# Kernel tuning notes

Hardware: AMD Instinct MI355X
Metric: run time of the kernel (lower is better)

The kernel has to match this reference:

```python
import jax, jax.numpy as jnp
import numpy as np

K = 3        # prediction_steps
SKIP = 1     # skip_step (forward default)
NEG = 64     # opt.negative_samples
EPS = 1e-11  # ExpNLLLoss epsilon


def setup_inputs() -> dict:
    key = jax.random.key(0)
    ks = jax.random.split(key, 8)
    B, C, H, W = 64, 256, 14, 14
    z = jax.random.normal(ks[0], (B, C, H, W), jnp.float32)
    c = jax.random.normal(ks[1], (B, C, H, W), jnp.float32)
    Wk = jax.random.normal(ks[2], (K, C, C), jnp.float32) / np.sqrt(C).astype(np.float32)
    inp = {"z": z, "c": c, "Wk": Wk}
    for k in range(1, K + 1):
        Hp = H - (k + SKIP)
        rows = Hp * W * B
        inp[f"neg_idx_k{k}"] = jax.random.randint(ks[2 + k], (rows * NEG,), 0, rows, dtype=jnp.int32)
    return inp


def _loss_k(z, c, Wk, neg_idx, k):
    # z, c: [B,C,H,W]; Wk: [Co,Ci] (1x1 conv); neg_idx: [(H-k-SKIP)*W*B*NEG]
    B, C, H, W = z.shape
    Hp = H - (k + SKIP)
    zt = z[:, :, k + SKIP:, :]                            # [B,Ci,Hp,W]
    ztwk = jnp.einsum('oc,bchw->hwbo', Wk, zt)            # [Hp,W,B,Co] (1x1 conv + permute(2,3,0,1))
    flat = ztwk.reshape(Hp * W * B, -1)
    shuf = flat[neg_idx].reshape(Hp, W, B, NEG, -1)       # gathered negatives [Hp,W,B,N,Co]
    ctx = jnp.transpose(c[:, :, :Hp, :], (2, 3, 0, 1))    # context c[:,:,:-(k+SKIP),:] -> [Hp,W,B,Co]
    main = jnp.einsum('hwbc,hwbc->hwb', ctx, ztwk)[..., None]   # [Hp,W,B,1]
    negs = jnp.einsum('hwbc,hwbnc->hwbn', ctx, shuf)            # [Hp,W,B,N]
    log_fk = jnp.concatenate([main, negs], axis=-1)             # [Hp,W,B,1+N]
    log_fk = jnp.transpose(log_fk, (2, 3, 0, 1))                # [B,1+N,Hp,W]
    probs = jax.nn.softmax(log_fk, axis=1)
    # ExpNLLLoss, target class 0, reduction='mean'
    return -jnp.mean(jnp.log(probs[:, 0] + EPS))


def reference(z, c, Wk, neg_idx_k1, neg_idx_k2, neg_idx_k3):
    idxs = [neg_idx_k1, neg_idx_k2, neg_idx_k3]
    total = 0.0
    for k in range(1, K + 1):
        total = total + _loss_k(z, c, Wk[k - 1], idxs[k - 1], k)
    return total / K
```

## Files before the change

kernel.cpp:

```cpp
#include <hip/hip_runtime.h>
#include <math.h>


typedef short bf16x8 __attribute__((ext_vector_type(8)));
typedef float f32x4 __attribute__((ext_vector_type(4)));

static __device__ __forceinline__ unsigned short f2bf(float f) {
    union { float f; unsigned int u; } x; x.f = f;
    unsigned int r = x.u + 0x7fffu + ((x.u >> 16) & 1u);
    return (unsigned short)(r >> 16);
}

static __device__ __forceinline__ unsigned char f2e4m3(float f) {
    union { float f; unsigned int u; } x; x.f = f;
    unsigned int s = (x.u >> 24) & 0x80u;
    float af = fabsf(f);
    if (af > 448.f) af = 448.f;
    x.f = af;
    unsigned int u = x.u;
    int e = (int)(u >> 23) - 127;
    unsigned int out;
    if (af == 0.f) {
        out = 0u;
    } else if (e < -6) {
        int mq = (int)rintf(af * 512.f);
        out = (mq >= 8) ? 0x08u : (unsigned int)mq;
    } else {
        unsigned int r = u + 0x7FFFFu + ((u >> 20) & 1u);
        int e2 = (int)(r >> 23) - 127;
        if (e2 > 8) out = 0x7Eu;
        else out = (unsigned int)(((e2 + 7) << 3) | ((r >> 20) & 7u));
    }
    return (unsigned char)(s | out);
}

static __device__ __forceinline__ void gload_lds4(const void* g, void* l) {
    __builtin_amdgcn_global_load_lds(
        (const __attribute__((address_space(1))) void*)g,
        (__attribute__((address_space(3))) void*)l, 4, 0, 0);
}

__global__ __launch_bounds__(256)
void prep_kernel(const float* __restrict__ z, const float* __restrict__ c,
                 const float* __restrict__ Wk,
                 unsigned short* __restrict__ zt, unsigned char* __restrict__ ct8,
                 unsigned short* __restrict__ wkb, float* __restrict__ out) {
    __shared__ float tile[16][201];
    const int tid = threadIdx.x;
    int x = blockIdx.x;
    if (x < 768) {
        int i = x * 256 + tid;
        wkb[i] = f2bf(Wk[i]);
        if (x == 0 && tid == 0) out[0] = 0.f;
        return;
    }
    const bool isz = x < 1792;
    const int local = isz ? (x - 768) : (x - 1792);
    const float* src = isz ? z : c;
    const int b  = local & 63;
    const int c0 = (local >> 6) << 4;
    for (int i = tid; i < 16 * 196; i += 256) {
        int cc = i / 196;
        int hw = i - cc * 196;
        tile[cc][hw] = src[(size_t)((b << 8) + c0 + cc) * 196 + hw];
    }
    __syncthreads();
    if (isz) {
        for (int i = tid; i < 196 * 16; i += 256) {
            int hw = i >> 4, cc = i & 15;
            zt[(size_t)((hw << 6) + b) * 256 + c0 + cc] = f2bf(tile[cc][hw]);
        }
    } else {
        for (int i = tid; i < 196 * 16; i += 256) {
            int hw = i >> 4, cc = i & 15;
            ct8[(size_t)((hw << 6) + b) * 256 + c0 + cc] = f2e4m3(tile[cc][hw]);
        }
    }
}

#define PSTR 528
__global__ __launch_bounds__(256)
void proj_mfma_kernel(const unsigned short* __restrict__ zt,
                      const unsigned short* __restrict__ wkb,
                      unsigned char* __restrict__ ztwk) {
    __shared__ __align__(16) unsigned char smem[(64 + 32) * PSTR];
    unsigned char* smA = smem;
    unsigned char* smB = smem + 64 * PSTR;

    int x = blockIdx.y;
    int k, hw;
    if (x < 168)      { k = 0; hw = x; }
    else if (x < 322) { k = 1; hw = x - 168; }
    else              { k = 2; hw = x - 322; }
    const int o0 = blockIdx.x << 5;
    const int row0  = hw << 6;
    const int zrow0 = row0 + (((k + 2) * 14) << 6);
    unsigned char* zo = ztwk + (size_t)k * 10752 * 256;

    const int tid = threadIdx.x;
    const unsigned char* zsrc = (const unsigned char*)(zt + (size_t)zrow0 * 256);
    const unsigned char* bsrc = (const unsigned char*)(wkb + ((size_t)k << 16) + o0 * 256);

    #pragma unroll
    for (int i = 0; i < 8; ++i) {
        int sb = ((i << 8) + tid) << 4;
        int r = sb >> 9, off = sb & 511;
        *(int4*)(smA + r * PSTR + off) = *(const int4*)(zsrc + sb);
    }
    #pragma unroll
    for (int i = 0; i < 4; ++i) {
        int sb = ((i << 8) + tid) << 4;
        int r = sb >> 9, off = sb & 511;
        *(int4*)(smB + r * PSTR + off) = *(const int4*)(bsrc + sb);
    }
    __syncthreads();

    const int wv = tid >> 6, lane = tid & 63;
    const int m = lane & 15, kq = lane >> 4;
    f32x4 acc[2] = {};
    const unsigned short* aP  = (const unsigned short*)(smA + (size_t)((wv << 4) + m) * PSTR) + (kq << 3);
    const unsigned short* bP0 = (const unsigned short*)(smB + (size_t)m * PSTR) + (kq << 3);
    const unsigned short* bP1 = (const unsigned short*)(smB + (size_t)(16 + m) * PSTR) + (kq << 3);
    #pragma unroll
    for (int kk = 0; kk < 256; kk += 32) {
        bf16x8 af = *(const bf16x8*)(aP  + kk);
        bf16x8 b0 = *(const bf16x8*)(bP0 + kk);
        bf16x8 b1 = *(const bf16x8*)(bP1 + kk);
        acc[0] = __builtin_amdgcn_mfma_f32_16x16x32_bf16(af, b0, acc[0], 0, 0, 0);
        acc[1] = __builtin_amdgcn_mfma_f32_16x16x32_bf16(af, b1, acc[1], 0, 0, 0);
    }
    __syncthreads();
    unsigned char* cs = smA;
    #pragma unroll
    for (int nt = 0; nt < 2; ++nt)
        #pragma unroll
        for (int r = 0; r < 4; ++r)
            cs[(size_t)((wv << 4) + (kq << 2) + r) * 40 + (nt << 4) + m] =
                f2e4m3(acc[nt][r]);
    __syncthreads();
    {
        int r = tid >> 2, off = (tid & 3) << 3;
        unsigned long long v = *(const unsigned long long*)(cs + (size_t)r * 40 + off);
        *(unsigned long long*)(zo + (size_t)(row0 + r) * 256 + o0 + off) = v;
    }
}

#define ROWB 272
__global__ __launch_bounds__(128, 4)
void loss_mfma_kernel(const unsigned char* __restrict__ ct8,
                      const unsigned char* __restrict__ ztwk8,
                      const int* __restrict__ n0, const int* __restrict__ n1,
                      const int* __restrict__ n2, float* __restrict__ rowloss) {
    __shared__ __align__(16) unsigned char slab[65 * ROWB];
    __shared__ __align__(16) unsigned char ctx_s[256];
    __shared__ float sred[2][2];
    const int tid = threadIdx.x;
    const int wv = tid >> 6, lane = tid & 63;
    const int m = lane & 15, kq = lane >> 4;

    int x = blockIdx.x;
    int k; const int* nb_base;
    if (x < 10752)      { k = 0; nb_base = n0; }
    else if (x < 20608) { k = 1; nb_base = n1; x -= 10752; }
    else                { k = 2; nb_base = n2; x -= 20608; }
    const int row = x;
    const unsigned char* flat8 = ztwk8 + (size_t)k * 10752 * 256;
    const float wk = (k == 0) ? (1.f / (3.f * 10752.f))
                   : (k == 1) ? (1.f / (3.f * 9856.f))
                              : (1.f / (3.f * 8960.f));
    const int rbase = (k == 0) ? 0 : (k == 1) ? 10752 : 20608;

    const int myidx = nb_base[((size_t)row << 6) + lane];

    if (wv == 0) {
        gload_lds4(flat8 + (size_t)row * 256 + (lane << 2), slab);
        #pragma unroll
        for (int j = 1; j <= 32; ++j) {
            int idx = __builtin_amdgcn_readlane(myidx, j - 1);
            gload_lds4(flat8 + (size_t)idx * 256 + (lane << 2), slab + j * ROWB);
        }
    } else {
        gload_lds4(ct8 + (size_t)row * 256 + (lane << 2), ctx_s);
        #pragma unroll
        for (int j = 33; j <= 64; ++j) {
            int idx = __builtin_amdgcn_readlane(myidx, j - 1);
            gload_lds4(flat8 + (size_t)idx * 256 + (lane << 2), slab + j * ROWB);
        }
    }
    __syncthreads();

    f32x4 acc[3] = {};
    const int mt0 = (wv == 0) ? 0 : 3;
    int soff[3];
    #pragma unroll
    for (int t = 0; t < 3; ++t) {
        int slot = ((mt0 + t) << 4) + m;
        if (slot > 64) slot = 64;
        soff[t] = slot * ROWB + (kq << 3);
    }
    const unsigned char* cp = ctx_s + (kq << 3);
    #pragma unroll
    for (int kk = 0; kk < 8; ++kk) {
        long long bfrag = *(const long long*)(cp + (kk << 5));
        #pragma unroll
        for (int t = 0; t < 3; ++t) {
            if (t < 2 || wv == 0) {
                long long af = *(const long long*)(slab + soff[t] + (kk << 5));
                acc[t] = __builtin_amdgcn_mfma_f32_16x16x32_fp8_fp8(af, bfrag, acc[t], 0, 0, 0);
            }
        }
    }

    float m_l = -1e30f;
    if (wv == 0) {
        #pragma unroll
        for (int t = 0; t < 3; ++t)
            #pragma unroll
            for (int r = 0; r < 4; ++r) m_l = fmaxf(m_l, acc[t][r]);
    } else {
        #pragma unroll
        for (int r = 0; r < 4; ++r) m_l = fmaxf(m_l, acc[0][r]);
        if (kq == 0) m_l = fmaxf(m_l, acc[1][0]);
    }
    m_l = fmaxf(m_l, __shfl_xor(m_l, 16));
    m_l = fmaxf(m_l, __shfl_xor(m_l, 32));

    float s_l = 0.f;
    if (wv == 0) {
        #pragma unroll
        for (int t = 0; t < 3; ++t)
            #pragma unroll
            for (int r = 0; r < 4; ++r) s_l += __expf(acc[t][r] - m_l);
    } else {
        #pragma unroll
        for (int r = 0; r < 4; ++r) s_l += __expf(acc[0][r] - m_l);
        if (kq == 0) s_l += __expf(acc[1][0] - m_l);
    }
    s_l += __shfl_xor(s_l, 16);
    s_l += __shfl_xor(s_l, 32);

    float main_l = acc[0][0];
    if (lane == 0) { sred[wv][0] = m_l; sred[wv][1] = s_l; }
    __syncthreads();
    if (tid == 0) {
        float m0 = sred[0][0], s0 = sred[0][1];
        float m1 = sred[1][0], s1 = sred[1][1];
        float mg = fmaxf(m0, m1);
        float sg = s0 * __expf(m0 - mg) + s1 * __expf(m1 - mg);
        float p0 = __expf(main_l - mg) / sg;
        rowloss[rbase + row] = -logf(p0 + 1e-11f) * wk;
    }
}

__global__ __launch_bounds__(256)
void reduce_kernel(const float* __restrict__ rl, float* __restrict__ out) {
    float s = 0.f;
    const int stride = gridDim.x * blockDim.x;
    for (int i = blockIdx.x * blockDim.x + threadIdx.x; i < 29568; i += stride)
        s += rl[i];
    #pragma unroll
    for (int off = 32; off >= 1; off >>= 1) s += __shfl_xor(s, off);
    if ((threadIdx.x & 63) == 0) atomicAdd(out, s);
}

extern "C" void kernel_launch(void* const* d_in, const int* in_sizes, int n_in,
                              void* d_out, int out_size, void* d_ws, size_t ws_size,
                              hipStream_t stream) {
    const float* z  = (const float*)d_in[0];
    const float* c  = (const float*)d_in[1];
    const float* Wk = (const float*)d_in[2];
    const int* negs[3] = {(const int*)d_in[3], (const int*)d_in[4], (const int*)d_in[5]};
    float* out = (float*)d_out;

    char* p = (char*)d_ws;
    unsigned short* zt      = (unsigned short*)p;   p += (size_t)196 * 64 * 256 * 2;
    unsigned short* wkb     = (unsigned short*)p;   p += (size_t)3 * 65536 * 2;
    unsigned char*  ct8     = (unsigned char*)p;    p += (size_t)196 * 64 * 256;
    unsigned char*  ztwk8   = (unsigned char*)p;    p += (size_t)3 * 10752 * 256;
    float*          rowloss = (float*)p;

    prep_kernel<<<2816, 256, 0, stream>>>(z, c, Wk, zt, ct8, wkb, out);
    proj_mfma_kernel<<<dim3(8, 462), 256, 0, stream>>>(zt, wkb, ztwk8);
    loss_mfma_kernel<<<29568, 128, 0, stream>>>(ct8, ztwk8, negs[0], negs[1],
                                                negs[2], rowloss);
    reduce_kernel<<<32, 256, 0, stream>>>(rowloss, out);
}
```

Before: 155.2 us.

## Restructure projection GEMM to keep A rows in registers and loop over output tiles

The projection kernel now gives each block 16 rows of z and all 256 output channels, instead of 64 rows by 32 channels. The A fragments stay in registers while the kernel loops over eight weight tiles staged through shared memory. The grid changes from 8x462 blocks of 256 threads to 1848 blocks of 128 threads. This cuts repeated loading of z rows across output-channel blocks, but each block reloads the whole weight matrix, does more syncs, and writes single fp8 bytes per lane instead of coalesced 8-byte stores.

```diff
diff --git a/kernel.cpp b/kernel.cpp
--- a/kernel.cpp
+++ b/kernel.cpp
@@ -78,70 +78,61 @@
     }
 }
 
-#define PSTR 528
-__global__ __launch_bounds__(256)
+#define QSTR 528
+__global__ __launch_bounds__(128, 4)
 void proj_mfma_kernel(const unsigned short* __restrict__ zt,
                       const unsigned short* __restrict__ wkb,
-                      unsigned char* __restrict__ ztwk) {
-    __shared__ __align__(16) unsigned char smem[(64 + 32) * PSTR];
-    unsigned char* smA = smem;
-    unsigned char* smB = smem + 64 * PSTR;
-
-    int x = blockIdx.y;
-    int k, hw;
-    if (x < 168)      { k = 0; hw = x; }
-    else if (x < 322) { k = 1; hw = x - 168; }
-    else              { k = 2; hw = x - 322; }
-    const int o0 = blockIdx.x << 5;
-    const int row0  = hw << 6;
-    const int zrow0 = row0 + (((k + 2) * 14) << 6);
-    unsigned char* zo = ztwk + (size_t)k * 10752 * 256;
-
+                      unsigned char* __restrict__ ztwk8) {
+    __shared__ __align__(16) unsigned char L[2 * 16 * QSTR];
     const int tid = threadIdx.x;
-    const unsigned char* zsrc = (const unsigned char*)(zt + (size_t)zrow0 * 256);
-    const unsigned char* bsrc = (const unsigned char*)(wkb + ((size_t)k << 16) + o0 * 256);
-
-    #pragma unroll
-    for (int i = 0; i < 8; ++i) {
-        int sb = ((i << 8) + tid) << 4;
-        int r = sb >> 9, off = sb & 511;
-        *(int4*)(smA + r * PSTR + off) = *(const int4*)(zsrc + sb);
-    }
-    #pragma unroll
-    for (int i = 0; i < 4; ++i) {
-        int sb = ((i << 8) + tid) << 4;
-        int r = sb >> 9, off = sb & 511;
-        *(int4*)(smB + r * PSTR + off) = *(const int4*)(bsrc + sb);
-    }
-    __syncthreads();
-
     const int wv = tid >> 6, lane = tid & 63;
     const int m = lane & 15, kq = lane >> 4;
-    f32x4 acc[2] = {};
-    const unsigned short* aP  = (const unsigned short*)(smA + (size_t)((wv << 4) + m) * PSTR) + (kq << 3);
-    const unsigned short* bP0 = (const unsigned short*)(smB + (size_t)m * PSTR) + (kq << 3);
-    const unsigned short* bP1 = (const unsigned short*)(smB + (size_t)(16 + m) * PSTR) + (kq << 3);
-    #pragma unroll
-    for (int kk = 0; kk < 256; kk += 32) {
-        bf16x8 af = *(const bf16x8*)(aP  + kk);
-        bf16x8 b0 = *(const bf16x8*)(bP0 + kk);
-        bf16x8 b1 = *(const bf16x8*)(bP1 + kk);
-        acc[0] = __builtin_amdgcn_mfma_f32_16x16x32_bf16(af, b0, acc[0], 0, 0, 0);
-        acc[1] = __builtin_amdgcn_mfma_f32_16x16x32_bf16(af, b1, acc[1], 0, 0, 0);
-    }
-    __syncthreads();
-    unsigned char* cs = smA;
-    #pragma unroll
-    for (int nt = 0; nt < 2; ++nt)
+
+    const int u = blockIdx.x;
+    int k, lt;
+    if (u < 672)       { k = 0; lt = u; }
+    else if (u < 1288) { k = 1; lt = u - 672; }
+    else               { k = 2; lt = u - 1288; }
+    const int row0  = lt << 4;
+    const int zrow0 = row0 + (k + 2) * 896;
+    unsigned char* zo = ztwk8 + (size_t)k * 10752 * 256;
+    const unsigned char* zsrc = (const unsigned char*)zt + (size_t)zrow0 * 512;
+    const unsigned char* wsrc = (const unsigned char*)wkb + (size_t)k * 131072;
+
+    for (int i = tid; i < 512; i += 128) {
+        int sb = i << 4;
+        int r = sb >> 9, off = sb & 511;
+        *(int4*)(L + r * QSTR + off) = *(const int4*)(zsrc + sb);
+    }
+    __syncthreads();
+    bf16x8 af[8];
+    #pragma unroll
+    for (int kk = 0; kk < 8; ++kk)
+        af[kk] = *(const bf16x8*)(L + m * QSTR + (kq << 4) + (kk << 6));
+    __syncthreads();
+
+    for (int it = 0; it < 8; ++it) {
+        for (int i = tid; i < 1024; i += 128) {
+            int sb = i << 4;
+            int t2 = sb >> 13;
+            int rem = sb & 8191;
+            int r = rem >> 9, off = rem & 511;
+            *(int4*)(L + t2 * 16 * QSTR + r * QSTR + off) =
+                *(const int4*)(wsrc + (size_t)(((it << 1) + t2) * 16 + r) * 512 + off);
+        }
+        __syncthreads();
+        const int o0 = ((it << 1) + wv) << 4;
+        const unsigned char* bb = L + wv * 16 * QSTR;
+        f32x4 acc = {0.f, 0.f, 0.f, 0.f};
+        #pragma unroll
+        for (int kk = 0; kk < 8; ++kk) {
+            bf16x8 bf = *(const bf16x8*)(bb + m * QSTR + (kq << 4) + (kk << 6));
+            acc = __builtin_amdgcn_mfma_f32_16x16x32_bf16(af[kk], bf, acc, 0, 0, 0);
+        }
         #pragma unroll
         for (int r = 0; r < 4; ++r)
-            cs[(size_t)((wv << 4) + (kq << 2) + r) * 40 + (nt << 4) + m] =
-                f2e4m3(acc[nt][r]);
-    __syncthreads();
-    {
-        int r = tid >> 2, off = (tid & 3) << 3;
-        unsigned long long v = *(const unsigned long long*)(cs + (size_t)r * 40 + off);
-        *(unsigned long long*)(zo + (size_t)(row0 + r) * 256 + o0 + off) = v;
+            zo[(size_t)(row0 + (kq << 2) + r) * 256 + o0 + m] = f2e4m3(acc[r]);
+        __syncthreads();
     }
 }
 
@@ -280,7 +271,7 @@
     float*          rowloss = (float*)p;
 
     prep_kernel<<<2816, 256, 0, stream>>>(z, c, Wk, zt, ct8, wkb, out);
-    proj_mfma_kernel<<<dim3(8, 462), 256, 0, stream>>>(zt, wkb, ztwk8);
+    proj_mfma_kernel<<<1848, 128, 0, stream>>>(zt, wkb, ztwk8);
     loss_mfma_kernel<<<29568, 128, 0, stream>>>(ct8, ztwk8, negs[0], negs[1],
                                                 negs[2], rowloss);
     reduce_kernel<<<32, 256, 0, stream>>>(rowloss, out);
```

New measurement: 164.7 us. 1.06x slower.
